# Performance work log

Measured on AMD Instinct MI355X. Metric: run time of the kernel, lower is better.

The kernel has to match this reference:

```python
import jax, jax.numpy as jnp
import numpy as np

B, C, H, W = 4, 64, 128, 128
O, K = 64, 3
STRIDE, PAD = 1, 1
K2 = K * K


def conv2d(x, w, b):
    out = jax.lax.conv_general_dilated(
        x, w, (STRIDE, STRIDE), [(PAD, PAD), (PAD, PAD)],
        dimension_numbers=('NCHW', 'OIHW', 'NCHW'))
    return out + b[None, :, None, None]


def setup_inputs() -> dict:
    key = jax.random.key(0)
    ks = jax.random.split(key, 6)
    return {
        'x': jax.random.normal(ks[0], (B, C, H, W), jnp.float32),
        'offset_w': jax.random.normal(ks[1], (2 * K2, C, K, K), jnp.float32) * 0.01,
        'offset_b': jax.random.normal(ks[2], (2 * K2,), jnp.float32) * 0.01,
        'mask_w': jax.random.normal(ks[3], (K2, C, K, K), jnp.float32) * 0.01,
        'mask_b': jnp.zeros((K2,), jnp.float32),
        'deform_w': jax.random.normal(ks[4], (O, C, K, K), jnp.float32) * (1.0 / np.sqrt(C * K2)),
        'deform_b': jax.random.normal(ks[5], (O,), jnp.float32) * 0.01,
    }


def _deform_conv(x, offset, mask, w, b):
    Bn, Cn, Hin, Win = x.shape
    Ho, Wo = offset.shape[2], offset.shape[3]
    off = offset.reshape(Bn, K2, 2, Ho, Wo)
    ky = jnp.repeat(jnp.arange(K), K)   # kernel row offset per location k
    kx = jnp.tile(jnp.arange(K), K)     # kernel col offset per location k
    yo = jnp.arange(Ho) * STRIDE - PAD
    xo = jnp.arange(Wo) * STRIDE - PAD
    # sampling positions [B,K2,Ho,Wo]
    py = off[:, :, 0] + ky[None, :, None, None] + yo[None, None, :, None]
    px = off[:, :, 1] + kx[None, :, None, None] + xo[None, None, None, :]
    y0 = jnp.floor(py)
    x0 = jnp.floor(px)
    wy1 = py - y0  # fractional weights
    wx1 = px - x0
    y0i = y0.astype(jnp.int32)
    x0i = x0.astype(jnp.int32)
    x_flat = x.reshape(Bn, Cn, Hin * Win)

    def corner(yi, xi, wgt):
        valid = (yi >= 0) & (yi < Hin) & (xi >= 0) & (xi < Win)
        yc = jnp.clip(yi, 0, Hin - 1)
        xc = jnp.clip(xi, 0, Win - 1)
        idx = (yc * Win + xc).reshape(Bn, -1)
        g = jnp.take_along_axis(x_flat, idx[:, None, :], axis=2)
        g = g.reshape(Bn, Cn, K2, Ho, Wo)
        return g * (wgt * valid)[:, None]

    val = (corner(y0i, x0i, (1 - wy1) * (1 - wx1))
           + corner(y0i, x0i + 1, (1 - wy1) * wx1)
           + corner(y0i + 1, x0i, wy1 * (1 - wx1))
           + corner(y0i + 1, x0i + 1, wy1 * wx1))
    val = val * mask[:, None]  # modulate, broadcast over channels
    out = jnp.einsum('bckhw,ock->bohw', val, w.reshape(w.shape[0], Cn, K2))
    return out + b[None, :, None, None]


def reference(x, offset_w, offset_b, mask_w, mask_b, deform_w, deform_b):
    offset = conv2d(x, offset_w, offset_b)
    mask = jax.nn.sigmoid(conv2d(x, mask_w, mask_b))
    return _deform_conv(x, offset, mask, deform_w, deform_b)
```

## Files before the change

kernel.cpp:

```cpp
#include <hip/hip_runtime.h>
#include <hip/hip_bf16.h>
#include <math.h>

#define BB 4
#define CC 64
#define HH 128
#define WW 128
#define HW 16384
#define CHW (CC*HW)

typedef __bf16 bf16;
typedef __attribute__((ext_vector_type(8))) __bf16 bf16x8;
typedef __attribute__((ext_vector_type(4))) __bf16 bf16x4;
typedef __attribute__((ext_vector_type(4))) float f32x4;
typedef __attribute__((ext_vector_type(4))) unsigned short u16x4;

#define MFMA(a, b, c) __builtin_amdgcn_mfma_f32_16x16x32_bf16((a), (b), (c), 0, 0, 0)

__global__ __launch_bounds__(256) void k_pre(const float* __restrict__ x,
        bf16* __restrict__ xt,
        const float* __restrict__ dw, const float* __restrict__ ow,
        const float* __restrict__ mw,
        bf16* __restrict__ wfd_hi, bf16* __restrict__ wfd_lo,
        bf16* __restrict__ wfo_hi, bf16* __restrict__ wfo_lo) {
    __shared__ float tile[64][65];
    if (blockIdx.x < 1024) {
        int b    = blockIdx.x >> 8;
        int s0   = (blockIdx.x & 255) * 64;
        int lane = threadIdx.x & 63;
        int w    = threadIdx.x >> 6;
        const float* xb = x + (size_t)b * CHW;
        #pragma unroll
        for (int r = 0; r < 16; ++r) {
            int c = w * 16 + r;
            tile[c][lane] = xb[(size_t)c * HW + s0 + lane];
        }
        __syncthreads();
        bf16* xtb = xt + (size_t)b * CHW;
        #pragma unroll
        for (int it = 0; it < 2; ++it) {
            int task = it * 256 + threadIdx.x;
            int s = task >> 3, ch0 = (task & 7) * 8;
            bf16x8 v;
            #pragma unroll
            for (int j = 0; j < 8; ++j) v[j] = (bf16)tile[ch0 + j][s];
            *(bf16x8*)&xtb[(size_t)(s0 + s) * 64 + ch0] = v;
        }
    } else {
        int idx = (blockIdx.x - 1024) * 256 + threadIdx.x;
        if (idx < 36864) {
            int j    = idx & 7;
            int lane = (idx >> 3) & 63;
            int ks   = (idx >> 9) % 18;
            int nt   = idx / (512 * 18);
            int n    = nt * 16 + (lane & 15);
            int kglob = ks * 32 + (lane >> 4) * 8 + j;
            int kk = kglob >> 6, c = kglob & 63;
            float w = dw[(n * 64 + c) * 9 + kk];
            bf16 h = (bf16)w;
            wfd_hi[idx] = h;
            wfd_lo[idx] = (bf16)(w - (float)h);
        } else {
            int idx2 = idx - 36864;
            int j    = idx2 & 7;
            int lane = (idx2 >> 3) & 63;
            int ks   = (idx2 >> 9) % 18;
            int nt   = idx2 / (512 * 18);
            int ch   = nt * 16 + (lane & 15);
            int kglob = ks * 32 + (lane >> 4) * 8 + j;
            int kk = kglob >> 6, c = kglob & 63;
            float w = 0.0f;
            if (ch < 18)      w = ow[(ch * 64 + c) * 9 + kk];
            else if (ch < 27) w = mw[((ch - 18) * 64 + c) * 9 + kk];
            bf16 h = (bf16)w;
            wfo_hi[idx2] = h;
            wfo_lo[idx2] = (bf16)(w - (float)h);
        }
    }
}

__global__ __launch_bounds__(256) void k_fused(const bf16* __restrict__ xt,
        const bf16* __restrict__ wfo_hi, const bf16* __restrict__ wfo_lo,
        const bf16* __restrict__ wfd_hi,
        const float* __restrict__ ob, const float* __restrict__ mb,
        const float* __restrict__ db, float* __restrict__ out) {
    __shared__ __align__(16) float om_s[4 * 27 * 16];
    __shared__ __align__(8)  bf16 sampw[4 * 144 * 4];
    __shared__ __align__(8)  unsigned short sampo[4 * 144 * 4];

    int bid = (blockIdx.x & 7) * 128 + (blockIdx.x >> 3);
    int pos0 = bid * 64;
    int wo0 = pos0 & 127;
    int ho  = (pos0 >> 7) & 127;
    int b   = pos0 >> 14;
    int t = threadIdx.x, wave = t >> 6, lane = t & 63;
    int m = lane & 15, g = lane >> 4;
    int st = wave;
    const bf16* xtb = xt + (size_t)b * CHW;
    float* omw = om_s + wave * 27 * 16;
    bf16* swv = sampw + wave * 144 * 4;
    unsigned short* sov = sampo + wave * 144 * 4;

    {
        f32x4 acc0 = {0.f, 0.f, 0.f, 0.f};
        f32x4 acc1 = {0.f, 0.f, 0.f, 0.f};
        const bf16x8* bh0 = (const bf16x8*)wfo_hi + lane;
        const bf16x8* bl0 = (const bf16x8*)wfo_lo + lane;
        const bf16x8* bh1 = (const bf16x8*)wfo_hi + 18 * 64 + lane;
        const bf16x8* bl1 = (const bf16x8*)wfo_lo + 18 * 64 + lane;
        #pragma unroll
        for (int kk = 0; kk < 9; ++kk) {
            int y  = ho + kk / 3 - 1;
            int xx = wo0 + st * 16 + m + (kk % 3) - 1;
            bf16x8 ae = {};
            bf16x8 ao = {};
            if ((unsigned)y < 128u && (unsigned)xx < 128u) {
                const bf16* bp = xtb + ((size_t)(y * 128 + xx) << 6);
                ae = *(const bf16x8*)(bp + g * 8);
                ao = *(const bf16x8*)(bp + 32 + g * 8);
            }
            int ks0 = 2 * kk, ks1 = 2 * kk + 1;
            acc0 = MFMA(ae, bh0[ks0 * 64], acc0);
            acc0 = MFMA(ae, bl0[ks0 * 64], acc0);
            acc0 = MFMA(ao, bh0[ks1 * 64], acc0);
            acc0 = MFMA(ao, bl0[ks1 * 64], acc0);
            acc1 = MFMA(ae, bh1[ks0 * 64], acc1);
            acc1 = MFMA(ae, bl1[ks0 * 64], acc1);
            acc1 = MFMA(ao, bh1[ks1 * 64], acc1);
            acc1 = MFMA(ao, bl1[ks1 * 64], acc1);
        }
        float bias0 = ob[m];
        f32x4 v0;
        #pragma unroll
        for (int r = 0; r < 4; ++r) v0[r] = acc0[r] + bias0;
        *(f32x4*)&omw[m * 16 + g * 4] = v0;
        int ch1 = 16 + m;
        if (ch1 < 27) {
            float bias1 = (ch1 < 18) ? ob[ch1] : mb[ch1 - 18];
            f32x4 v1;
            #pragma unroll
            for (int r = 0; r < 4; ++r) {
                float v = acc1[r] + bias1;
                if (ch1 >= 18) v = 1.0f / (1.0f + __expf(-v));
                v1[r] = v;
            }
            *(f32x4*)&omw[ch1 * 16 + g * 4] = v1;
        }
    }
    asm volatile("s_waitcnt lgkmcnt(0)" ::: "memory");

    #pragma unroll
    for (int i = 0; i < 3; ++i) {
        int task = i * 64 + lane;
        if (task < 144) {
            int p = task / 9, k = task - p * 9;
            float dy = omw[(2 * k) * 16 + p];
            float dx = omw[(2 * k + 1) * 16 + p];
            float mk = omw[(18 + k) * 16 + p];
            float py = (float)(ho - 1 + k / 3) + dy;
            float px = (float)(wo0 + st * 16 + p - 1 + (k % 3)) + dx;
            float y0f = floorf(py), x0f = floorf(px);
            float fy = py - y0f, fx = px - x0f;
            int y0 = (int)y0f, x0 = (int)x0f;
            int y1 = y0 + 1,  x1 = x0 + 1;
            bool vy0 = (unsigned)y0 < 128u, vy1 = (unsigned)y1 < 128u;
            bool vx0 = (unsigned)x0 < 128u, vx1 = (unsigned)x1 < 128u;
            int y0c = min(max(y0, 0), 127), y1c = min(max(y1, 0), 127);
            int x0c = min(max(x0, 0), 127), x1c = min(max(x1, 0), 127);
            bf16x4 wv;
            wv.x = (bf16)((vy0 && vx0) ? mk * (1.f - fy) * (1.f - fx) : 0.f);
            wv.y = (bf16)((vy0 && vx1) ? mk * (1.f - fy) * fx         : 0.f);
            wv.z = (bf16)((vy1 && vx0) ? mk * fy * (1.f - fx)         : 0.f);
            wv.w = (bf16)((vy1 && vx1) ? mk * fy * fx                 : 0.f);
            u16x4 ov;
            ov.x = (unsigned short)(y0c * 128 + x0c);
            ov.y = (unsigned short)(y0c * 128 + x1c);
            ov.z = (unsigned short)(y1c * 128 + x0c);
            ov.w = (unsigned short)(y1c * 128 + x1c);
            *(bf16x4*)&swv[task * 4] = wv;
            *(u16x4*)&sov[task * 4] = ov;
        }
    }
    asm volatile("s_waitcnt lgkmcnt(0)" ::: "memory");

    const bf16x8* bfd = (const bf16x8*)wfd_hi + lane;
    f32x4 acc[4];
    #pragma unroll
    for (int nt = 0; nt < 4; ++nt) acc[nt] = (f32x4){0.f, 0.f, 0.f, 0.f};
    int sb = m * 9 * 4;
    #pragma unroll 3
    for (int kk = 0; kk < 9; ++kk) {
        bf16x4 wb = *(const bf16x4*)&swv[sb + kk * 4];
        u16x4  o4 = *(const u16x4*)&sov[sb + kk * 4];
        const bf16* p00 = xtb + (((int)o4.x) << 6) + g * 8;
        const bf16* p01 = xtb + (((int)o4.y) << 6) + g * 8;
        const bf16* p10 = xtb + (((int)o4.z) << 6) + g * 8;
        const bf16* p11 = xtb + (((int)o4.w) << 6) + g * 8;
        bf16x8 v00a = *(const bf16x8*)p00, v00b = *(const bf16x8*)(p00 + 32);
        bf16x8 v01a = *(const bf16x8*)p01, v01b = *(const bf16x8*)(p01 + 32);
        bf16x8 v10a = *(const bf16x8*)p10, v10b = *(const bf16x8*)(p10 + 32);
        bf16x8 v11a = *(const bf16x8*)p11, v11b = *(const bf16x8*)(p11 + 32);
        float w00 = (float)wb.x, w01 = (float)wb.y;
        float w10 = (float)wb.z, w11 = (float)wb.w;
        bf16x8 af0, af1;
        #pragma unroll
        for (int j = 0; j < 8; ++j) {
            af0[j] = (bf16)(w00 * (float)v00a[j] + w01 * (float)v01a[j]
                          + w10 * (float)v10a[j] + w11 * (float)v11a[j]);
            af1[j] = (bf16)(w00 * (float)v00b[j] + w01 * (float)v01b[j]
                          + w10 * (float)v10b[j] + w11 * (float)v11b[j]);
        }
        int ks0 = 2 * kk, ks1 = 2 * kk + 1;
        acc[0] = MFMA(af0, bfd[(0 * 18 + ks0) * 64], acc[0]);
        acc[0] = MFMA(af1, bfd[(0 * 18 + ks1) * 64], acc[0]);
        acc[1] = MFMA(af0, bfd[(1 * 18 + ks0) * 64], acc[1]);
        acc[1] = MFMA(af1, bfd[(1 * 18 + ks1) * 64], acc[1]);
        acc[2] = MFMA(af0, bfd[(2 * 18 + ks0) * 64], acc[2]);
        acc[2] = MFMA(af1, bfd[(2 * 18 + ks1) * 64], acc[2]);
        acc[3] = MFMA(af0, bfd[(3 * 18 + ks0) * 64], acc[3]);
        acc[3] = MFMA(af1, bfd[(3 * 18 + ks1) * 64], acc[3]);
    }
    #pragma unroll
    for (int nt = 0; nt < 4; ++nt) {
        int o = nt * 16 + m;
        float bias = db[o];
        float4 vv = {acc[nt][0] + bias, acc[nt][1] + bias,
                     acc[nt][2] + bias, acc[nt][3] + bias};
        *(float4*)&out[((size_t)(b * 64 + o)) * HW + ho * 128 + wo0 + st * 16 + g * 4] = vv;
    }
}

extern "C" void kernel_launch(void* const* d_in, const int* in_sizes, int n_in,
                              void* d_out, int out_size, void* d_ws, size_t ws_size,
                              hipStream_t stream) {
    const float* x   = (const float*)d_in[0];
    const float* ow  = (const float*)d_in[1];
    const float* ob  = (const float*)d_in[2];
    const float* mw  = (const float*)d_in[3];
    const float* mb  = (const float*)d_in[4];
    const float* db  = (const float*)d_in[6];
    const float* dw  = (const float*)d_in[5];
    float* out = (float*)d_out;

    bf16* xt = (bf16*)d_ws;
    bf16* wfd_hi = xt + (size_t)BB * HW * CC;
    bf16* wfd_lo = wfd_hi + 36864;
    bf16* wfo_hi = wfd_lo + 36864;
    bf16* wfo_lo = wfo_hi + 18432;

    k_pre<<<1024 + 216, 256, 0, stream>>>(x, xt, dw, ow, mw, wfd_hi, wfd_lo, wfo_hi, wfo_lo);
    k_fused<<<(BB * HW) / 64, 256, 0, stream>>>(xt, wfo_hi, wfo_lo, wfd_hi, ob, mb, db, out);
}
```

Measured before the change: 138.9 us.

## Split kernel-position reduction across wave pairs with LDS partial-sum combine

```diff
diff --git a/kernel.cpp b/kernel.cpp
--- a/kernel.cpp
+++ b/kernel.cpp
@@ -79,11 +79,12 @@
     }
 }
 
-__global__ __launch_bounds__(256) void k_fused(const bf16* __restrict__ xt,
+__global__ __launch_bounds__(512, 8) void k_fused(const bf16* __restrict__ xt,
         const bf16* __restrict__ wfo_hi, const bf16* __restrict__ wfo_lo,
         const bf16* __restrict__ wfd_hi,
         const float* __restrict__ ob, const float* __restrict__ mb,
         const float* __restrict__ db, float* __restrict__ out) {
+    __shared__ __align__(16) char scratch_s[4 * 4096];
     __shared__ __align__(16) float om_s[4 * 27 * 16];
     __shared__ __align__(8)  bf16 sampw[4 * 144 * 4];
     __shared__ __align__(8)  unsigned short sampo[4 * 144 * 4];
@@ -94,22 +95,22 @@
     int ho  = (pos0 >> 7) & 127;
     int b   = pos0 >> 14;
     int t = threadIdx.x, wave = t >> 6, lane = t & 63;
+    int pair = wave >> 1, half = wave & 1;
+    int st = pair;
     int m = lane & 15, g = lane >> 4;
-    int st = wave;
     const bf16* xtb = xt + (size_t)b * CHW;
-    float* omw = om_s + wave * 27 * 16;
-    bf16* swv = sampw + wave * 144 * 4;
-    unsigned short* sov = sampo + wave * 144 * 4;
-
+
+    f32x4 acc0 = {0.f, 0.f, 0.f, 0.f};
+    f32x4 acc1 = {0.f, 0.f, 0.f, 0.f};
     {
-        f32x4 acc0 = {0.f, 0.f, 0.f, 0.f};
-        f32x4 acc1 = {0.f, 0.f, 0.f, 0.f};
         const bf16x8* bh0 = (const bf16x8*)wfo_hi + lane;
         const bf16x8* bl0 = (const bf16x8*)wfo_lo + lane;
         const bf16x8* bh1 = (const bf16x8*)wfo_hi + 18 * 64 + lane;
         const bf16x8* bl1 = (const bf16x8*)wfo_lo + 18 * 64 + lane;
-        #pragma unroll
-        for (int kk = 0; kk < 9; ++kk) {
+        int nB  = half ? 4 : 5;
+        int kkB = half ? 5 : 0;
+        for (int i = 0; i < nB; ++i) {
+            int kk = kkB + i;
             int y  = ho + kk / 3 - 1;
             int xx = wo0 + st * 16 + m + (kk % 3) - 1;
             bf16x8 ae = {};
@@ -129,26 +130,41 @@
             acc1 = MFMA(ao, bh1[ks1 * 64], acc1);
             acc1 = MFMA(ao, bl1[ks1 * 64], acc1);
         }
+    }
+    int ch1 = 16 + m;
+    {
+        float* op = (float*)(scratch_s + pair * 4096 + half * 1728);
+        *(f32x4*)&op[m * 16 + g * 4] = acc0;
+        if (ch1 < 27) *(f32x4*)&op[ch1 * 16 + g * 4] = acc1;
+    }
+    __syncthreads();
+
+    float* omw = om_s + pair * 27 * 16;
+    {
+        const float* pp = (const float*)(scratch_s + pair * 4096 + (half ^ 1) * 1728);
+        f32x4 p0 = *(const f32x4*)&pp[m * 16 + g * 4];
         float bias0 = ob[m];
         f32x4 v0;
         #pragma unroll
-        for (int r = 0; r < 4; ++r) v0[r] = acc0[r] + bias0;
+        for (int r = 0; r < 4; ++r) v0[r] = acc0[r] + p0[r] + bias0;
         *(f32x4*)&omw[m * 16 + g * 4] = v0;
-        int ch1 = 16 + m;
         if (ch1 < 27) {
+            f32x4 p1 = *(const f32x4*)&pp[ch1 * 16 + g * 4];
             float bias1 = (ch1 < 18) ? ob[ch1] : mb[ch1 - 18];
             f32x4 v1;
             #pragma unroll
             for (int r = 0; r < 4; ++r) {
-                float v = acc1[r] + bias1;
+                float v = acc1[r] + p1[r] + bias1;
                 if (ch1 >= 18) v = 1.0f / (1.0f + __expf(-v));
                 v1[r] = v;
             }
             *(f32x4*)&omw[ch1 * 16 + g * 4] = v1;
         }
     }
-    asm volatile("s_waitcnt lgkmcnt(0)" ::: "memory");
-
+    __syncthreads();
+
+    bf16* swv = sampw + pair * 144 * 4;
+    unsigned short* sov = sampo + pair * 144 * 4;
     #pragma unroll
     for (int i = 0; i < 3; ++i) {
         int task = i * 64 + lane;
@@ -188,28 +204,47 @@
     #pragma unroll
     for (int nt = 0; nt < 4; ++nt) acc[nt] = (f32x4){0.f, 0.f, 0.f, 0.f};
     int sb = m * 9 * 4;
-    #pragma unroll 3
-    for (int kk = 0; kk < 9; ++kk) {
+    int nD  = half ? 5 : 4;
+    int kkD = half ? 0 : 5;
+    for (int i = 0; i < nD; ++i) {
+        int kk = kkD + i;
         bf16x4 wb = *(const bf16x4*)&swv[sb + kk * 4];
         u16x4  o4 = *(const u16x4*)&sov[sb + kk * 4];
         const bf16* p00 = xtb + (((int)o4.x) << 6) + g * 8;
         const bf16* p01 = xtb + (((int)o4.y) << 6) + g * 8;
         const bf16* p10 = xtb + (((int)o4.z) << 6) + g * 8;
         const bf16* p11 = xtb + (((int)o4.w) << 6) + g * 8;
-        bf16x8 v00a = *(const bf16x8*)p00, v00b = *(const bf16x8*)(p00 + 32);
-        bf16x8 v01a = *(const bf16x8*)p01, v01b = *(const bf16x8*)(p01 + 32);
-        bf16x8 v10a = *(const bf16x8*)p10, v10b = *(const bf16x8*)(p10 + 32);
-        bf16x8 v11a = *(const bf16x8*)p11, v11b = *(const bf16x8*)(p11 + 32);
         float w00 = (float)wb.x, w01 = (float)wb.y;
         float w10 = (float)wb.z, w11 = (float)wb.w;
+        float f0[8], f1[8];
+        bf16x8 v;
+        v = *(const bf16x8*)p00;
+        #pragma unroll
+        for (int j = 0; j < 8; ++j) f0[j] = w00 * (float)v[j];
+        v = *(const bf16x8*)(p00 + 32);
+        #pragma unroll
+        for (int j = 0; j < 8; ++j) f1[j] = w00 * (float)v[j];
+        v = *(const bf16x8*)p01;
+        #pragma unroll
+        for (int j = 0; j < 8; ++j) f0[j] += w01 * (float)v[j];
+        v = *(const bf16x8*)(p01 + 32);
+        #pragma unroll
+        for (int j = 0; j < 8; ++j) f1[j] += w01 * (float)v[j];
+        v = *(const bf16x8*)p10;
+        #pragma unroll
+        for (int j = 0; j < 8; ++j) f0[j] += w10 * (float)v[j];
+        v = *(const bf16x8*)(p10 + 32);
+        #pragma unroll
+        for (int j = 0; j < 8; ++j) f1[j] += w10 * (float)v[j];
+        v = *(const bf16x8*)p11;
+        #pragma unroll
+        for (int j = 0; j < 8; ++j) f0[j] += w11 * (float)v[j];
+        v = *(const bf16x8*)(p11 + 32);
+        #pragma unroll
+        for (int j = 0; j < 8; ++j) f1[j] += w11 * (float)v[j];
         bf16x8 af0, af1;
         #pragma unroll
-        for (int j = 0; j < 8; ++j) {
-            af0[j] = (bf16)(w00 * (float)v00a[j] + w01 * (float)v01a[j]
-                          + w10 * (float)v10a[j] + w11 * (float)v11a[j]);
-            af1[j] = (bf16)(w00 * (float)v00b[j] + w01 * (float)v01b[j]
-                          + w10 * (float)v10b[j] + w11 * (float)v11b[j]);
-        }
+        for (int j = 0; j < 8; ++j) { af0[j] = (bf16)f0[j]; af1[j] = (bf16)f1[j]; }
         int ks0 = 2 * kk, ks1 = 2 * kk + 1;
         acc[0] = MFMA(af0, bfd[(0 * 18 + ks0) * 64], acc[0]);
         acc[0] = MFMA(af1, bfd[(0 * 18 + ks1) * 64], acc[0]);
@@ -220,13 +255,24 @@
         acc[3] = MFMA(af0, bfd[(3 * 18 + ks0) * 64], acc[3]);
         acc[3] = MFMA(af1, bfd[(3 * 18 + ks1) * 64], acc[3]);
     }
-    #pragma unroll
-    for (int nt = 0; nt < 4; ++nt) {
-        int o = nt * 16 + m;
-        float bias = db[o];
-        float4 vv = {acc[nt][0] + bias, acc[nt][1] + bias,
-                     acc[nt][2] + bias, acc[nt][3] + bias};
-        *(float4*)&out[((size_t)(b * 64 + o)) * HW + ho * 128 + wo0 + st * 16 + g * 4] = vv;
+
+    float* dre = (float*)(scratch_s + pair * 4096);
+    if (half) {
+        #pragma unroll
+        for (int nt = 0; nt < 4; ++nt)
+            *(f32x4*)&dre[nt * 256 + lane * 4] = acc[nt];
+    }
+    __syncthreads();
+    if (!half) {
+        #pragma unroll
+        for (int nt = 0; nt < 4; ++nt) {
+            f32x4 pa = *(const f32x4*)&dre[nt * 256 + lane * 4];
+            int o = nt * 16 + m;
+            float bias = db[o];
+            float4 vv = {acc[nt][0] + pa[0] + bias, acc[nt][1] + pa[1] + bias,
+                         acc[nt][2] + pa[2] + bias, acc[nt][3] + pa[3] + bias};
+            *(float4*)&out[((size_t)(b * 64 + o)) * HW + ho * 128 + wo0 + st * 16 + g * 4] = vv;
+        }
     }
 }
 
@@ -238,8 +284,8 @@
     const float* ob  = (const float*)d_in[2];
     const float* mw  = (const float*)d_in[3];
     const float* mb  = (const float*)d_in[4];
+    const float* dw  = (const float*)d_in[5];
     const float* db  = (const float*)d_in[6];
-    const float* dw  = (const float*)d_in[5];
     float* out = (float*)d_out;
 
     bf16* xt = (bf16*)d_ws;
@@ -249,5 +295,5 @@
     bf16* wfo_lo = wfo_hi + 18432;
 
     k_pre<<<1024 + 216, 256, 0, stream>>>(x, xt, dw, ow, mw, wfd_hi, wfd_lo, wfo_hi, wfo_lo);
-    k_fused<<<(BB * HW) / 64, 256, 0, stream>>>(xt, wfo_hi, wfo_lo, wfd_hi, ob, mb, db, out);
+    k_fused<<<(BB * HW) / 64, 512, 0, stream>>>(xt, wfo_hi, wfo_lo, wfd_hi, ob, mb, db, out);
 }
```

Result: slower. 148.3 us (+6.7%).
